# Performance work log

Measured on AMD Instinct MI355X. Metric: run time of the kernel, lower is better.

## Reference

```python
import jax, jax.numpy as jnp
import numpy as np

N_NODES = 50000
N_EDGES = 800000
D_NODE = 64
HID = 64
N_TGT = 64


def _init_linear(key, fan_in, fan_out):
    # torch.nn.Linear default init: U(-1/sqrt(fan_in), 1/sqrt(fan_in))
    kw, kb = jax.random.split(key)
    bound = 1.0 / np.sqrt(fan_in)
    W = jax.random.uniform(kw, (fan_in, fan_out), minval=-bound, maxval=bound, dtype=jnp.float32)
    b = jax.random.uniform(kb, (fan_out,), minval=-bound, maxval=bound, dtype=jnp.float32)
    return W, b


def setup_inputs() -> dict:
    key = jax.random.key(0)
    ks = jax.random.split(key, 8)
    x = jax.random.normal(ks[0], (N_NODES, D_NODE), dtype=jnp.float32)
    edge_index = jax.random.randint(ks[1], (2, N_EDGES), 0, N_NODES, dtype=jnp.int64)
    edge_attr = jax.random.normal(ks[2], (N_EDGES, HID), dtype=jnp.float32)
    u = jax.random.normal(ks[3], (1, 16), dtype=jnp.float32)
    batch = jnp.zeros((N_NODES,), dtype=jnp.int64)
    W1a, b1a = _init_linear(ks[4], D_NODE + HID, HID)
    W1b, b1b = _init_linear(ks[5], HID, HID)
    W2a, b2a = _init_linear(ks[6], D_NODE + HID, HID)
    W2b, b2b = _init_linear(ks[7], HID, N_TGT)
    return {"x": x, "edge_index": edge_index, "edge_attr": edge_attr, "u": u,
            "batch": batch,
            "W1a": W1a, "b1a": b1a, "W1b": W1b, "b1b": b1b,
            "W2a": W2a, "b2a": b2a, "W2b": W2b, "b2b": b2b}


def reference(x, edge_index, edge_attr, u, batch,
              W1a, b1a, W1b, b1b, W2a, b2a, W2b, b2b):
    row, col = edge_index[0], edge_index[1]
    # per-edge: gather target-node feats + edge attrs -> MLP1
    msg = jnp.concatenate([x[col], edge_attr], axis=1)          # [E, D+H]
    msg = jnp.maximum(msg @ W1a + b1a, 0.0) @ W1b + b1b          # [E, H]
    # scatter_mean over source nodes
    summed = jax.ops.segment_sum(msg, row, num_segments=x.shape[0])   # [N, H]
    counts = jax.ops.segment_sum(jnp.ones((row.shape[0],), msg.dtype), row,
                                 num_segments=x.shape[0])             # [N]
    agg = summed / jnp.maximum(counts, 1.0)[:, None]
    # per-node: concat + MLP2
    h = jnp.concatenate([x, agg], axis=1)                        # [N, D+H]
    out = jnp.maximum(h @ W2a + b2a, 0.0) @ W2b + b2b            # [N, T]
    return out
```

## Files before the change

### kernel.cpp

```cpp
#include <hip/hip_runtime.h>
#include <hip/hip_bf16.h>

#define NN 50000
#define NE 800000

typedef __attribute__((ext_vector_type(8))) short short8;
typedef __attribute__((ext_vector_type(4))) float f32x4;

static __device__ __forceinline__ short f2bf(float f) {
    __hip_bfloat16 h = __float2bfloat16(f);
    return __builtin_bit_cast(short, h);
}

static __device__ __forceinline__ short8 cvt8(f32x4 a, f32x4 b) {
    short8 v;
    v[0] = f2bf(a[0]); v[1] = f2bf(a[1]); v[2] = f2bf(a[2]); v[3] = f2bf(a[3]);
    v[4] = f2bf(b[0]); v[5] = f2bf(b[1]); v[6] = f2bf(b[2]); v[7] = f2bf(b[3]);
    return v;
}

#define LOAD_BFRAGS(W, FR, KT)                                        \
    _Pragma("unroll")                                                 \
    for (int t = 0; t < (KT); ++t) {                                  \
        _Pragma("unroll")                                             \
        for (int nt = 0; nt < 4; ++nt) {                              \
            short8 v;                                                 \
            _Pragma("unroll")                                         \
            for (int i = 0; i < 8; ++i)                               \
                v[i] = f2bf((W)[(32*t + 8*g + i)*64 + 16*nt + er]);   \
            FR[t][nt] = v;                                            \
        }                                                             \
    }

__global__ __launch_bounds__(256, 2) void edge_kernel(
    const float* __restrict__ x, const int* __restrict__ ei,
    const float* __restrict__ ea,
    const float* __restrict__ W1a, const float* __restrict__ b1a,
    const float* __restrict__ W1b, const float* __restrict__ b1b,
    float* __restrict__ summed, float* __restrict__ counts)
{
    __shared__ short h1s[4][16*64];
    const int tid  = threadIdx.x;
    const int wid  = tid >> 6;
    const int lane = tid & 63;
    const int er   = lane & 15;
    const int g    = lane >> 4;
    short* myh1 = h1s[wid];

    short8 Wa[4][4];
    short8 Wb[2][4];
    LOAD_BFRAGS(W1a, Wa, 4)
    LOAD_BFRAGS(W1b, Wb, 2)
    float bias1[4], bias2[4];
    #pragma unroll
    for (int nt = 0; nt < 4; ++nt) { bias1[nt] = b1a[16*nt + er]; bias2[nt] = b1b[16*nt + er]; }

    for (int tile = blockIdx.x * 4 + wid; tile < NE/16; tile += gridDim.x * 4) {
        const int eb  = tile * 16;
        const int col = ei[NE + eb + er];
        const float* xr = x  + (size_t)col * 64;
        const float* qr = ea + (size_t)(eb + er) * 64;

        short8 A[4];
        #pragma unroll
        for (int t = 0; t < 2; ++t) {
            f32x4 v0 = *(const f32x4*)(xr + 32*t + 8*g);
            f32x4 v1 = *(const f32x4*)(xr + 32*t + 8*g + 4);
            A[t] = cvt8(v0, v1);
        }
        #pragma unroll
        for (int t = 0; t < 2; ++t) {
            f32x4 v0 = *(const f32x4*)(qr + 32*t + 8*g);
            f32x4 v1 = *(const f32x4*)(qr + 32*t + 8*g + 4);
            A[2+t] = cvt8(v0, v1);
        }

        f32x4 acc[4] = {{0,0,0,0},{0,0,0,0},{0,0,0,0},{0,0,0,0}};
        #pragma unroll
        for (int t = 0; t < 4; ++t)
            #pragma unroll
            for (int nt = 0; nt < 4; ++nt)
                acc[nt] = __builtin_amdgcn_mfma_f32_16x16x32_bf16(A[t], Wa[t][nt], acc[nt], 0, 0, 0);

        #pragma unroll
        for (int r = 0; r < 4; ++r) {
            const int e = 4*g + r;
            const int swz = (e & 7) << 3;
            #pragma unroll
            for (int nt = 0; nt < 4; ++nt) {
                float h = acc[nt][r] + bias1[nt];
                h = h > 0.0f ? h : 0.0f;
                myh1[e*64 + ((16*nt + er) ^ swz)] = f2bf(h);
            }
        }

        const int swr = (er & 7) << 3;
        short8 A2[2];
        #pragma unroll
        for (int t = 0; t < 2; ++t)
            A2[t] = *(const short8*)(myh1 + er*64 + ((32*t + 8*g) ^ swr));

        f32x4 acc2[4] = {{0,0,0,0},{0,0,0,0},{0,0,0,0},{0,0,0,0}};
        #pragma unroll
        for (int t = 0; t < 2; ++t)
            #pragma unroll
            for (int nt = 0; nt < 4; ++nt)
                acc2[nt] = __builtin_amdgcn_mfma_f32_16x16x32_bf16(A2[t], Wb[t][nt], acc2[nt], 0, 0, 0);

        #pragma unroll
        for (int r = 0; r < 4; ++r) {
            const int rid = ei[eb + 4*g + r];
            float* dst = summed + (size_t)rid * 64 + er;
            #pragma unroll
            for (int nt = 0; nt < 4; ++nt)
                atomicAdd(dst + 16*nt, acc2[nt][r] + bias2[nt]);
        }
        if (g == 0)
            atomicAdd(counts + ei[eb + er], 1.0f);
    }
}

__global__ __launch_bounds__(256, 2) void node_kernel(
    const float* __restrict__ x, const float* __restrict__ counts,
    const float* __restrict__ W2a, const float* __restrict__ b2a,
    const float* __restrict__ W2b, const float* __restrict__ b2b,
    float* out )
{
    __shared__ short h1s[4][16*64];
    const int tid  = threadIdx.x;
    const int wid  = tid >> 6;
    const int lane = tid & 63;
    const int er   = lane & 15;
    const int g    = lane >> 4;
    short* myh1 = h1s[wid];

    short8 Wa[4][4];
    short8 Wb[2][4];
    LOAD_BFRAGS(W2a, Wa, 4)
    LOAD_BFRAGS(W2b, Wb, 2)
    float bias1[4], bias2[4];
    #pragma unroll
    for (int nt = 0; nt < 4; ++nt) { bias1[nt] = b2a[16*nt + er]; bias2[nt] = b2b[16*nt + er]; }

    const int tile = blockIdx.x * 4 + wid;
    if (tile >= NN/16) return;
    const int nb   = tile * 16;
    const int node = nb + er;

    const float* xr = x   + (size_t)node * 64;
    const float* sr = out + (size_t)node * 64;
    const float  c  = counts[node];
    const float  rc = 1.0f / fmaxf(c, 1.0f);

    short8 A[4];
    #pragma unroll
    for (int t = 0; t < 2; ++t) {
        f32x4 v0 = *(const f32x4*)(xr + 32*t + 8*g);
        f32x4 v1 = *(const f32x4*)(xr + 32*t + 8*g + 4);
        A[t] = cvt8(v0, v1);
    }
    #pragma unroll
    for (int t = 0; t < 2; ++t) {
        f32x4 v0 = *(const f32x4*)(sr + 32*t + 8*g);
        f32x4 v1 = *(const f32x4*)(sr + 32*t + 8*g + 4);
        v0 *= rc; v1 *= rc;
        A[2+t] = cvt8(v0, v1);
    }

    f32x4 acc[4] = {{0,0,0,0},{0,0,0,0},{0,0,0,0},{0,0,0,0}};
    #pragma unroll
    for (int t = 0; t < 4; ++t)
        #pragma unroll
        for (int nt = 0; nt < 4; ++nt)
            acc[nt] = __builtin_amdgcn_mfma_f32_16x16x32_bf16(A[t], Wa[t][nt], acc[nt], 0, 0, 0);

    #pragma unroll
    for (int r = 0; r < 4; ++r) {
        const int e = 4*g + r;
        const int swz = (e & 7) << 3;
        #pragma unroll
        for (int nt = 0; nt < 4; ++nt) {
            float h = acc[nt][r] + bias1[nt];
            h = h > 0.0f ? h : 0.0f;
            myh1[e*64 + ((16*nt + er) ^ swz)] = f2bf(h);
        }
    }

    const int swr = (er & 7) << 3;
    short8 A2[2];
    #pragma unroll
    for (int t = 0; t < 2; ++t)
        A2[t] = *(const short8*)(myh1 + er*64 + ((32*t + 8*g) ^ swr));

    f32x4 acc2[4] = {{0,0,0,0},{0,0,0,0},{0,0,0,0},{0,0,0,0}};
    #pragma unroll
    for (int t = 0; t < 2; ++t)
        #pragma unroll
        for (int nt = 0; nt < 4; ++nt)
            acc2[nt] = __builtin_amdgcn_mfma_f32_16x16x32_bf16(A2[t], Wb[t][nt], acc2[nt], 0, 0, 0);

    #pragma unroll
    for (int r = 0; r < 4; ++r) {
        float* orow = out + (size_t)(nb + 4*g + r) * 64 + er;
        #pragma unroll
        for (int nt = 0; nt < 4; ++nt)
            orow[16*nt] = acc2[nt][r] + bias2[nt];
    }
}

extern "C" void kernel_launch(void* const* d_in, const int* in_sizes, int n_in,
                              void* d_out, int out_size, void* d_ws, size_t ws_size,
                              hipStream_t stream)
{
    const float* x   = (const float*)d_in[0];
    const int*   ei  = (const int*)d_in[1];
    const float* ea  = (const float*)d_in[2];
    const float* W1a = (const float*)d_in[5];
    const float* b1a = (const float*)d_in[6];
    const float* W1b = (const float*)d_in[7];
    const float* b1b = (const float*)d_in[8];
    const float* W2a = (const float*)d_in[9];
    const float* b2a = (const float*)d_in[10];
    const float* W2b = (const float*)d_in[11];
    const float* b2b = (const float*)d_in[12];

    float* out    = (float*)d_out;
    float* counts = (float*)d_ws;

    hipMemsetAsync(out,    0, (size_t)NN * 64 * sizeof(float), stream);
    hipMemsetAsync(counts, 0, (size_t)NN * sizeof(float),      stream);

    edge_kernel<<<3125, 256, 0, stream>>>(x, ei, ea, W1a, b1a, W1b, b1b, out, counts);
    node_kernel<<<782, 256, 0, stream>>>(x, counts, W2a, b2a, W2b, b2b, out);
}
```

Before: 488.1 us.

## Accumulate edge messages with packed bf16 atomics into a workspace buffer

```diff
diff --git a/kernel.cpp b/kernel.cpp
--- a/kernel.cpp
+++ b/kernel.cpp
@@ -5,6 +5,7 @@
 #define NE 800000
 
 typedef __attribute__((ext_vector_type(8))) short short8;
+typedef __attribute__((ext_vector_type(8))) unsigned short ushort8;
 typedef __attribute__((ext_vector_type(4))) float f32x4;
 
 static __device__ __forceinline__ short f2bf(float f) {
@@ -32,12 +33,13 @@
         }                                                             \
     }
 
-__global__ __launch_bounds__(256, 2) void edge_kernel(
+__global__ __launch_bounds__(256, 4) void edge_kernel(
     const float* __restrict__ x, const int* __restrict__ ei,
     const float* __restrict__ ea,
     const float* __restrict__ W1a, const float* __restrict__ b1a,
     const float* __restrict__ W1b, const float* __restrict__ b1b,
-    float* __restrict__ summed, float* __restrict__ counts)
+    unsigned short* __restrict__ summed ,
+    float* __restrict__ counts)
 {
     __shared__ short h1s[4][16*64];
     const int tid  = threadIdx.x;
@@ -110,10 +112,19 @@
         #pragma unroll
         for (int r = 0; r < 4; ++r) {
             const int rid = ei[eb + 4*g + r];
-            float* dst = summed + (size_t)rid * 64 + er;
-            #pragma unroll
-            for (int nt = 0; nt < 4; ++nt)
-                atomicAdd(dst + 16*nt, acc2[nt][r] + bias2[nt]);
+            #pragma unroll
+            for (int nt = 0; nt < 4; ++nt) {
+                float v = acc2[nt][r] + bias2[nt];
+                float o = __shfl_xor(v, 1);
+                if (!(er & 1)) {
+                    unsigned int pk = (unsigned int)(unsigned short)f2bf(v)
+                                    | ((unsigned int)(unsigned short)f2bf(o) << 16);
+                    unsigned short* dst = summed + (size_t)rid * 64 + 16*nt + er;
+                    asm volatile("global_atomic_pk_add_bf16 %0, %1, off"
+                                 :: "v"((unsigned long long)(uintptr_t)dst), "v"(pk)
+                                 : "memory");
+                }
+            }
         }
         if (g == 0)
             atomicAdd(counts + ei[eb + er], 1.0f);
@@ -121,10 +132,12 @@
 }
 
 __global__ __launch_bounds__(256, 2) void node_kernel(
-    const float* __restrict__ x, const float* __restrict__ counts,
+    const float* __restrict__ x,
+    const unsigned short* __restrict__ summed ,
+    const float* __restrict__ counts,
     const float* __restrict__ W2a, const float* __restrict__ b2a,
     const float* __restrict__ W2b, const float* __restrict__ b2b,
-    float* out )
+    float* __restrict__ out)
 {
     __shared__ short h1s[4][16*64];
     const int tid  = threadIdx.x;
@@ -147,8 +160,8 @@
     const int nb   = tile * 16;
     const int node = nb + er;
 
-    const float* xr = x   + (size_t)node * 64;
-    const float* sr = out + (size_t)node * 64;
+    const float* xr = x + (size_t)node * 64;
+    const unsigned short* sr = summed + (size_t)node * 64;
     const float  c  = counts[node];
     const float  rc = 1.0f / fmaxf(c, 1.0f);
 
@@ -161,10 +174,14 @@
     }
     #pragma unroll
     for (int t = 0; t < 2; ++t) {
-        f32x4 v0 = *(const f32x4*)(sr + 32*t + 8*g);
-        f32x4 v1 = *(const f32x4*)(sr + 32*t + 8*g + 4);
-        v0 *= rc; v1 *= rc;
-        A[2+t] = cvt8(v0, v1);
+        ushort8 s = *(const ushort8*)(sr + 32*t + 8*g);
+        short8 a;
+        #pragma unroll
+        for (int i = 0; i < 8; ++i) {
+            float f = __builtin_bit_cast(float, ((unsigned int)s[i]) << 16) * rc;
+            a[i] = f2bf(f);
+        }
+        A[2+t] = a;
     }
 
     f32x4 acc[4] = {{0,0,0,0},{0,0,0,0},{0,0,0,0},{0,0,0,0}};
@@ -224,12 +241,14 @@
     const float* W2b = (const float*)d_in[11];
     const float* b2b = (const float*)d_in[12];
 
-    float* out    = (float*)d_out;
-    float* counts = (float*)d_ws;
-
-    hipMemsetAsync(out,    0, (size_t)NN * 64 * sizeof(float), stream);
-    hipMemsetAsync(counts, 0, (size_t)NN * sizeof(float),      stream);
-
-    edge_kernel<<<3125, 256, 0, stream>>>(x, ei, ea, W1a, b1a, W1b, b1b, out, counts);
-    node_kernel<<<782, 256, 0, stream>>>(x, counts, W2a, b2a, W2b, b2b, out);
-}
+    float* out = (float*)d_out;
+
+    unsigned short* summed = (unsigned short*)d_ws;
+    float* counts = (float*)((char*)d_ws + (size_t)NN * 64 * sizeof(unsigned short));
+
+    hipMemsetAsync(d_ws, 0, (size_t)NN * 64 * sizeof(unsigned short)
+                          + (size_t)NN * sizeof(float), stream);
+
+    edge_kernel<<<6250, 256, 0, stream>>>(x, ei, ea, W1a, b1a, W1b, b1b, summed, counts);
+    node_kernel<<<782, 256, 0, stream>>>(x, summed, counts, W2a, b2a, W2b, b2b, out);
+}
```

Result: slower. 591.6 us (+21.2%).

## Replace scatter atomics with CSR-sorted per-node edge aggregation

Applied to the files above, without the earlier changes.

```diff
diff --git a/kernel.cpp b/kernel.cpp
--- a/kernel.cpp
+++ b/kernel.cpp
@@ -32,12 +32,46 @@
         }                                                             \
     }
 
-__global__ __launch_bounds__(256, 2) void edge_kernel(
+__global__ void hist_kernel(const int* __restrict__ ei, int* __restrict__ cnt) {
+    int e = blockIdx.x * 256 + threadIdx.x;
+    if (e < NE) atomicAdd(&cnt[ei[e]], 1);
+}
+
+__global__ void scan_kernel(const int* __restrict__ cnt,
+                            int* __restrict__ off, int* __restrict__ cursor) {
+    __shared__ int sums[256];
+    const int t = threadIdx.x;
+    const int base = t * 196;
+    int s = 0;
+    for (int i = 0; i < 196; ++i) { int idx = base + i; if (idx < NN) s += cnt[idx]; }
+    sums[t] = s; __syncthreads();
+    for (int d = 1; d < 256; d <<= 1) {
+        int u = (t >= d) ? sums[t - d] : 0;
+        __syncthreads();
+        sums[t] += u;
+        __syncthreads();
+    }
+    int run = sums[t] - s;
+    for (int i = 0; i < 196; ++i) {
+        int idx = base + i;
+        if (idx < NN) { off[idx] = run; cursor[idx] = run; run += cnt[idx]; }
+    }
+    if (t == 255) off[NN] = run;
+}
+
+__global__ void fill_kernel(const int* __restrict__ ei,
+                            int* __restrict__ cursor, int* __restrict__ elist) {
+    int e = blockIdx.x * 256 + threadIdx.x;
+    if (e < NE) { int p = atomicAdd(&cursor[ei[e]], 1); elist[p] = e; }
+}
+
+__global__ __launch_bounds__(256, 2) void edge_agg_kernel(
     const float* __restrict__ x, const int* __restrict__ ei,
     const float* __restrict__ ea,
+    const int* __restrict__ off, const int* __restrict__ elist,
     const float* __restrict__ W1a, const float* __restrict__ b1a,
     const float* __restrict__ W1b, const float* __restrict__ b1b,
-    float* __restrict__ summed, float* __restrict__ counts)
+    float* __restrict__ agg )
 {
     __shared__ short h1s[4][16*64];
     const int tid  = threadIdx.x;
@@ -55,73 +89,85 @@
     #pragma unroll
     for (int nt = 0; nt < 4; ++nt) { bias1[nt] = b1a[16*nt + er]; bias2[nt] = b1b[16*nt + er]; }
 
-    for (int tile = blockIdx.x * 4 + wid; tile < NE/16; tile += gridDim.x * 4) {
-        const int eb  = tile * 16;
-        const int col = ei[NE + eb + er];
-        const float* xr = x  + (size_t)col * 64;
-        const float* qr = ea + (size_t)(eb + er) * 64;
-
-        short8 A[4];
-        #pragma unroll
-        for (int t = 0; t < 2; ++t) {
-            f32x4 v0 = *(const f32x4*)(xr + 32*t + 8*g);
-            f32x4 v1 = *(const f32x4*)(xr + 32*t + 8*g + 4);
-            A[t] = cvt8(v0, v1);
+    for (int n = blockIdx.x * 4 + wid; n < NN; n += gridDim.x * 4) {
+        const int o0  = off[n];
+        const int deg = off[n + 1] - o0;
+        float psum[4] = {0.f, 0.f, 0.f, 0.f};
+
+        for (int c0 = 0; c0 < deg; c0 += 16) {
+            const int eid = elist[(c0 + er < deg) ? (o0 + c0 + er) : o0];
+            const int col = ei[NE + eid];
+            const float* xr = x  + (size_t)col * 64;
+            const float* qr = ea + (size_t)eid * 64;
+
+            short8 A[4];
+            #pragma unroll
+            for (int t = 0; t < 2; ++t) {
+                f32x4 v0 = *(const f32x4*)(xr + 32*t + 8*g);
+                f32x4 v1 = *(const f32x4*)(xr + 32*t + 8*g + 4);
+                A[t] = cvt8(v0, v1);
+            }
+            #pragma unroll
+            for (int t = 0; t < 2; ++t) {
+                f32x4 v0 = *(const f32x4*)(qr + 32*t + 8*g);
+                f32x4 v1 = *(const f32x4*)(qr + 32*t + 8*g + 4);
+                A[2+t] = cvt8(v0, v1);
+            }
+
+            f32x4 acc[4] = {{0,0,0,0},{0,0,0,0},{0,0,0,0},{0,0,0,0}};
+            #pragma unroll
+            for (int t = 0; t < 4; ++t)
+                #pragma unroll
+                for (int nt = 0; nt < 4; ++nt)
+                    acc[nt] = __builtin_amdgcn_mfma_f32_16x16x32_bf16(A[t], Wa[t][nt], acc[nt], 0, 0, 0);
+
+            #pragma unroll
+            for (int r = 0; r < 4; ++r) {
+                const int e = 4*g + r;
+                const int swz = (e & 7) << 3;
+                #pragma unroll
+                for (int nt = 0; nt < 4; ++nt) {
+                    float h = acc[nt][r] + bias1[nt];
+                    h = h > 0.0f ? h : 0.0f;
+                    myh1[e*64 + ((16*nt + er) ^ swz)] = f2bf(h);
+                }
+            }
+
+            const int swr = (er & 7) << 3;
+            short8 A2[2];
+            #pragma unroll
+            for (int t = 0; t < 2; ++t)
+                A2[t] = *(const short8*)(myh1 + er*64 + ((32*t + 8*g) ^ swr));
+
+            f32x4 acc2[4] = {{0,0,0,0},{0,0,0,0},{0,0,0,0},{0,0,0,0}};
+            #pragma unroll
+            for (int t = 0; t < 2; ++t)
+                #pragma unroll
+                for (int nt = 0; nt < 4; ++nt)
+                    acc2[nt] = __builtin_amdgcn_mfma_f32_16x16x32_bf16(A2[t], Wb[t][nt], acc2[nt], 0, 0, 0);
+
+            #pragma unroll
+            for (int r = 0; r < 4; ++r) {
+                const bool valid = (c0 + 4*g + r) < deg;
+                #pragma unroll
+                for (int nt = 0; nt < 4; ++nt)
+                    psum[nt] += valid ? (acc2[nt][r] + bias2[nt]) : 0.0f;
+            }
         }
-        #pragma unroll
-        for (int t = 0; t < 2; ++t) {
-            f32x4 v0 = *(const f32x4*)(qr + 32*t + 8*g);
-            f32x4 v1 = *(const f32x4*)(qr + 32*t + 8*g + 4);
-            A[2+t] = cvt8(v0, v1);
+
+        #pragma unroll
+        for (int nt = 0; nt < 4; ++nt) {
+            psum[nt] += __shfl_xor(psum[nt], 16);
+            psum[nt] += __shfl_xor(psum[nt], 32);
         }
-
-        f32x4 acc[4] = {{0,0,0,0},{0,0,0,0},{0,0,0,0},{0,0,0,0}};
-        #pragma unroll
-        for (int t = 0; t < 4; ++t)
-            #pragma unroll
-            for (int nt = 0; nt < 4; ++nt)
-                acc[nt] = __builtin_amdgcn_mfma_f32_16x16x32_bf16(A[t], Wa[t][nt], acc[nt], 0, 0, 0);
-
-        #pragma unroll
-        for (int r = 0; r < 4; ++r) {
-            const int e = 4*g + r;
-            const int swz = (e & 7) << 3;
-            #pragma unroll
-            for (int nt = 0; nt < 4; ++nt) {
-                float h = acc[nt][r] + bias1[nt];
-                h = h > 0.0f ? h : 0.0f;
-                myh1[e*64 + ((16*nt + er) ^ swz)] = f2bf(h);
-            }
-        }
-
-        const int swr = (er & 7) << 3;
-        short8 A2[2];
-        #pragma unroll
-        for (int t = 0; t < 2; ++t)
-            A2[t] = *(const short8*)(myh1 + er*64 + ((32*t + 8*g) ^ swr));
-
-        f32x4 acc2[4] = {{0,0,0,0},{0,0,0,0},{0,0,0,0},{0,0,0,0}};
-        #pragma unroll
-        for (int t = 0; t < 2; ++t)
-            #pragma unroll
-            for (int nt = 0; nt < 4; ++nt)
-                acc2[nt] = __builtin_amdgcn_mfma_f32_16x16x32_bf16(A2[t], Wb[t][nt], acc2[nt], 0, 0, 0);
-
-        #pragma unroll
-        for (int r = 0; r < 4; ++r) {
-            const int rid = ei[eb + 4*g + r];
-            float* dst = summed + (size_t)rid * 64 + er;
-            #pragma unroll
-            for (int nt = 0; nt < 4; ++nt)
-                atomicAdd(dst + 16*nt, acc2[nt][r] + bias2[nt]);
-        }
-        if (g == 0)
-            atomicAdd(counts + ei[eb + er], 1.0f);
+        float sel = (g == 0) ? psum[0] : (g == 1) ? psum[1] : (g == 2) ? psum[2] : psum[3];
+        const float rdeg = 1.0f / fmaxf((float)deg, 1.0f);
+        agg[(size_t)n * 64 + lane] = sel * rdeg;
     }
 }
 
 __global__ __launch_bounds__(256, 2) void node_kernel(
-    const float* __restrict__ x, const float* __restrict__ counts,
+    const float* __restrict__ x,
     const float* __restrict__ W2a, const float* __restrict__ b2a,
     const float* __restrict__ W2b, const float* __restrict__ b2b,
     float* out )
@@ -143,14 +189,12 @@
     for (int nt = 0; nt < 4; ++nt) { bias1[nt] = b2a[16*nt + er]; bias2[nt] = b2b[16*nt + er]; }
 
     const int tile = blockIdx.x * 4 + wid;
-    if (tile >= NN/16) return;
+    if (tile >= (NN + 15) / 16) return;
     const int nb   = tile * 16;
-    const int node = nb + er;
+    const int node = min(nb + er, NN - 1);
 
     const float* xr = x   + (size_t)node * 64;
     const float* sr = out + (size_t)node * 64;
-    const float  c  = counts[node];
-    const float  rc = 1.0f / fmaxf(c, 1.0f);
 
     short8 A[4];
     #pragma unroll
@@ -163,7 +207,6 @@
     for (int t = 0; t < 2; ++t) {
         f32x4 v0 = *(const f32x4*)(sr + 32*t + 8*g);
         f32x4 v1 = *(const f32x4*)(sr + 32*t + 8*g + 4);
-        v0 *= rc; v1 *= rc;
         A[2+t] = cvt8(v0, v1);
     }
 
@@ -224,12 +267,20 @@
     const float* W2b = (const float*)d_in[11];
     const float* b2b = (const float*)d_in[12];
 
-    float* out    = (float*)d_out;
-    float* counts = (float*)d_ws;
-
-    hipMemsetAsync(out,    0, (size_t)NN * 64 * sizeof(float), stream);
-    hipMemsetAsync(counts, 0, (size_t)NN * sizeof(float),      stream);
-
-    edge_kernel<<<3125, 256, 0, stream>>>(x, ei, ea, W1a, b1a, W1b, b1b, out, counts);
-    node_kernel<<<782, 256, 0, stream>>>(x, counts, W2a, b2a, W2b, b2b, out);
-}
+    float* out = (float*)d_out;
+
+    int* cnt    = (int*)d_ws;
+    int* off    = cnt + NN;
+    int* cursor = off + NN + 1;
+    int* elist  = cursor + NN;
+
+    hipMemsetAsync(cnt, 0, (size_t)NN * sizeof(int), stream);
+
+    hist_kernel<<<(NE + 255) / 256, 256, 0, stream>>>(ei, cnt);
+    scan_kernel<<<1, 256, 0, stream>>>(cnt, off, cursor);
+    fill_kernel<<<(NE + 255) / 256, 256, 0, stream>>>(ei, cursor, elist);
+
+    edge_agg_kernel<<<3125, 256, 0, stream>>>(x, ei, ea, off, elist,
+                                              W1a, b1a, W1b, b1b, out);
+    node_kernel<<<782, 256, 0, stream>>>(x, W2a, b2a, W2b, b2b, out);
+}
```

After: 681.5 us. +39.6%, slower.
